# Kernel optimization log

Hardware: AMD Instinct MI355X
Metric: run time of the kernel (lower is better)

## Reference

```python
import jax, jax.numpy as jnp
import numpy as np


def setup_inputs() -> dict:
    key = jax.random.key(0)
    k1, k2, k3, k4 = jax.random.split(key, 4)
    B, C, H, W = 8, 512, 64, 64  # h must equal w per the broadcast in the original
    opt = jax.random.normal(k1, (B, C, H, W), dtype=jnp.float32)
    sar = jax.random.normal(k2, (B, C, H, W), dtype=jnp.float32)
    # 1x1 conv weights, shape [out_c, in_c] (kernel spatial dims are 1x1)
    W_opt = jax.random.normal(k3, (C, C), dtype=jnp.float32) * (2.0 / C) ** 0.5
    W_sar = jax.random.normal(k4, (C, C), dtype=jnp.float32) * (2.0 / C) ** 0.5
    return {"opt": opt, "sar": sar, "W_opt": W_opt, "W_sar": W_sar}


def _branch(x, Wc):
    # 1x1 conv: per-pixel channel mixing. Q = K = V (same conv applied to same input).
    f = jnp.einsum('oc,bchw->bohw', Wc, x)            # (b,c,h,w)
    # S[b,c,i,j] = sum_h Q[b,c,h,i] * K[b,c,h,j]  (transpose(2,3) @ original)
    S = jnp.einsum('bchi,bchj->bcij', f, f)           # (b,c,w,w)
    # nn.Softmax() with no dim on 4D -> softmax over channel dim (axis=1)
    S = jax.nn.softmax(S, axis=1)
    return f, S


def reference(opt, sar, W_opt, W_sar):
    V_opt, S_opt = _branch(opt, W_opt)
    V_sar, S_sar = _branch(sar, W_sar)
    hadamard = S_opt * S_sar                          # (b,c,w,w); h==w lets it broadcast with V
    Att = (V_opt * hadamard) * (V_sar * hadamard)
    return Att
```

## Files before the change

kernel.cpp:

```cpp
#include <hip/hip_runtime.h>
#include <cstdint>

#define CCH 512
#define HW  4096
#define WDIM 64
#define NBATCH 8
#define CHW ((size_t)CCH * HW)

typedef __attribute__((ext_vector_type(8))) short bf16x8;
typedef __attribute__((ext_vector_type(4))) float f32x4;

__device__ __forceinline__ unsigned short f2bf(float x) {
  unsigned u = __float_as_uint(x);
  unsigned r = (u + 0x7FFFu + ((u >> 16) & 1u)) >> 16;
  return (unsigned short)r;
}
__device__ __forceinline__ float bf2f(unsigned short h) {
  return __uint_as_float(((unsigned)h) << 16);
}

__device__ __forceinline__ void gl_lds16(const void* g, void* l) {
  __builtin_amdgcn_global_load_lds(
      (const __attribute__((address_space(1))) void*)g,
      (__attribute__((address_space(3))) void*)l, 16, 0, 0);
}

__global__ __launch_bounds__(256) void wsplit_k(
    const float* __restrict__ Wo, const float* __restrict__ Wsr,
    unsigned short* __restrict__ Whl) {
  const int br = blockIdx.y;
  const float* W = br ? Wsr : Wo;
  const int i = blockIdx.x * 256 + threadIdx.x;
  const float x = W[i];
  const unsigned short h = f2bf(x);
  unsigned short* dst = Whl + (size_t)br * 524288;
  dst[i] = h;
  dst[262144 + i] = f2bf(x - bf2f(h));
}

__global__ __launch_bounds__(256, 4) void mfma_conv_k(
    const unsigned short* __restrict__ Whl,
    const float* __restrict__ opt, const float* __restrict__ sar,
    float* __restrict__ F, int b0) {
  const int z = blockIdx.z;
  const int br = z & 1, bl = z >> 1;
  const unsigned short* Ah_g = Whl + (size_t)br * 524288;
  const unsigned short* Al_g = Ah_g + 262144;
  const float* Xb = (br ? sar : opt) + (size_t)(b0 + bl) * CHW;
  const int n0 = blockIdx.x * 128, m0 = blockIdx.y * 128;

  __shared__ unsigned short Ahs[128 * 32];
  __shared__ unsigned short Als[128 * 32];
  __shared__ float Xs[32 * 128];

  const int tid = threadIdx.x;
  const int wave = tid >> 6, lane = tid & 63;
  const int wm = (wave >> 1) * 64, wn = (wave & 1) * 64;

  f32x4 acc[4][4] = {};

  const int rl = lane >> 2;
  const int kcA = (((lane & 3) ^ ((lane >> 3) & 3)) * 8);

  const int brow_off = wave * 2 + (lane >> 5);
  const int bcol = (lane & 31) * 4;

  const int fr = lane & 15;
  const int quad = lane >> 4;
  const int khA = ((quad ^ ((lane >> 1) & 3)) * 8);

  for (int k0 = 0; k0 < CCH; k0 += 32) {
    __syncthreads();
#pragma unroll
    for (int q = 0; q < 2; ++q) {
      const int rbase = wave * 32 + q * 16;
      const int r = rbase + rl;
      gl_lds16(Ah_g + (size_t)(m0 + r) * CCH + k0 + kcA, &Ahs[rbase * 32]);
      gl_lds16(Al_g + (size_t)(m0 + r) * CCH + k0 + kcA, &Als[rbase * 32]);
    }
#pragma unroll
    for (int t = 0; t < 4; ++t) {
      const int row = t * 8 + brow_off;
      const int srccol = (bcol + 128 - 8 * t) & 127;
      gl_lds16(&Xb[(size_t)(k0 + row) * HW + n0 + srccol],
               &Xs[t * 1024 + wave * 256]);
    }
    __syncthreads();

    bf16x8 ah[4], al[4];
#pragma unroll
    for (int i = 0; i < 4; ++i) {
      ah[i] = *(const bf16x8*)&Ahs[(wm + i * 16 + fr) * 32 + khA];
      al[i] = *(const bf16x8*)&Als[(wm + i * 16 + fr) * 32 + khA];
    }

#pragma unroll
    for (int j = 0; j < 4; ++j) {
      const int colj = (wn + j * 16 + fr + 8 * quad) & 127;
      unsigned short hs[8], ls[8];
#pragma unroll
      for (int s = 0; s < 8; ++s) {
        const float x = Xs[(quad * 8 + s) * 128 + colj];
        const unsigned xu = __float_as_uint(x);
        const float hi = __uint_as_float(xu & 0xFFFF0000u);
        const float lof = x - hi;
        hs[s] = (unsigned short)(xu >> 16);
        ls[s] = (unsigned short)(__float_as_uint(lof) >> 16);
      }
      const bf16x8 bh = *(const bf16x8*)hs;
      const bf16x8 bl = *(const bf16x8*)ls;
#pragma unroll
      for (int i = 0; i < 4; ++i) {
        acc[i][j] = __builtin_amdgcn_mfma_f32_16x16x32_bf16(ah[i], bh, acc[i][j], 0, 0, 0);
        acc[i][j] = __builtin_amdgcn_mfma_f32_16x16x32_bf16(ah[i], bl, acc[i][j], 0, 0, 0);
        acc[i][j] = __builtin_amdgcn_mfma_f32_16x16x32_bf16(al[i], bh, acc[i][j], 0, 0, 0);
      }
    }
  }

  float* Fb = F + (size_t)z * CHW;
  const int col = lane & 15, rq = (lane >> 4) * 4;
#pragma unroll
  for (int i = 0; i < 4; ++i)
#pragma unroll
    for (int j = 0; j < 4; ++j) {
      const int n = n0 + wn + j * 16 + col;
#pragma unroll
      for (int r = 0; r < 4; ++r) {
        const int m = m0 + wm + i * 16 + rq + r;
        Fb[(size_t)m * HW + n] = acc[i][j][r];
      }
    }
}

#define FT_S 72
__global__ __launch_bounds__(256, 4) void gram_k(
    const float* __restrict__ F, float* __restrict__ S) {
  const size_t base = ((size_t)blockIdx.y * CCH + blockIdx.x) * HW;
  const float* Fc = F + base;
  float* Sc = S + base;

  __shared__ float Fs[64][68];
  __shared__ unsigned short FtH[64 * FT_S];
  __shared__ unsigned short FtL[64 * FT_S];

  const int tid = threadIdx.x;

  {
    const int h = tid >> 2;
    const int w0 = (tid & 3) * 16;
    const float* src = &Fc[h * 64 + w0];
    float4 v0 = *(const float4*)(src + 0);
    float4 v1 = *(const float4*)(src + 4);
    float4 v2 = *(const float4*)(src + 8);
    float4 v3 = *(const float4*)(src + 12);
    *(float4*)&Fs[h][w0 + 0]  = v0;
    *(float4*)&Fs[h][w0 + 4]  = v1;
    *(float4*)&Fs[h][w0 + 8]  = v2;
    *(float4*)&Fs[h][w0 + 12] = v3;
  }
  __syncthreads();

  {
    const int w = tid & 63;
    const int hc = (tid >> 6) * 16;
    unsigned short hb[16], lb[16];
#pragma unroll
    for (int k = 0; k < 16; ++k) {
      const float x = Fs[hc + k][w];
      const unsigned short h = f2bf(x);
      hb[k] = h;
      lb[k] = f2bf(x - bf2f(h));
    }
    unsigned short* dh = &FtH[w * FT_S + hc];
    unsigned short* dl = &FtL[w * FT_S + hc];
    *(uint4*)(dh + 0) = *(uint4*)&hb[0];
    *(uint4*)(dh + 8) = *(uint4*)&hb[8];
    *(uint4*)(dl + 0) = *(uint4*)&lb[0];
    *(uint4*)(dl + 8) = *(uint4*)&lb[8];
  }
  __syncthreads();

  const int wave = tid >> 6, lane = tid & 63;
  const int wm = (wave >> 1) * 32, wn = (wave & 1) * 32;
  const int fr = lane & 15, kq = (lane >> 4) * 8;

  f32x4 acc[2][2] = {};
#pragma unroll
  for (int kcc = 0; kcc < 2; ++kcc) {
    bf16x8 ah[2], al[2], bh[2], bl[2];
#pragma unroll
    for (int i = 0; i < 2; ++i) {
      ah[i] = *(const bf16x8*)&FtH[(wm + i * 16 + fr) * FT_S + kcc * 32 + kq];
      al[i] = *(const bf16x8*)&FtL[(wm + i * 16 + fr) * FT_S + kcc * 32 + kq];
      bh[i] = *(const bf16x8*)&FtH[(wn + i * 16 + fr) * FT_S + kcc * 32 + kq];
      bl[i] = *(const bf16x8*)&FtL[(wn + i * 16 + fr) * FT_S + kcc * 32 + kq];
    }
#pragma unroll
    for (int i = 0; i < 2; ++i)
#pragma unroll
      for (int j = 0; j < 2; ++j) {
        acc[i][j] = __builtin_amdgcn_mfma_f32_16x16x32_bf16(ah[i], bh[j], acc[i][j], 0, 0, 0);
        acc[i][j] = __builtin_amdgcn_mfma_f32_16x16x32_bf16(ah[i], bl[j], acc[i][j], 0, 0, 0);
        acc[i][j] = __builtin_amdgcn_mfma_f32_16x16x32_bf16(al[i], bh[j], acc[i][j], 0, 0, 0);
      }
  }

  const int rq = (lane >> 4) * 4;
#pragma unroll
  for (int i = 0; i < 2; ++i)
#pragma unroll
    for (int j = 0; j < 2; ++j) {
      const int n = wn + j * 16 + fr;
#pragma unroll
      for (int r = 0; r < 4; ++r) {
        const int m = wm + i * 16 + rq + r;
        Sc[m * 64 + n] = acc[i][j][r];
      }
    }
}

__global__ __launch_bounds__(1024, 8) void softmax_fuse_k(
    const float* __restrict__ S, const float* __restrict__ Fbuf,
    float* __restrict__ Out) {
  const int i = blockIdx.x;
  const int b = blockIdx.y;
  const int tid = threadIdx.x;
  const int jl = (tid & 15) * 4;
  const int g = tid >> 4;

  const size_t rowO = (size_t)(b * 2) * CHW + (size_t)i * WDIM;
  const size_t rowS = rowO + CHW;

  float mo[4], lo[4], ms[4], ls[4];
#pragma unroll
  for (int k = 0; k < 4; ++k) { mo[k] = -1e30f; lo[k] = 0.f; ms[k] = -1e30f; ls[k] = 0.f; }

#pragma unroll
  for (int cc = 0; cc < 8; ++cc) {
    const int c = g * 8 + cc;
    const size_t off = (size_t)c * HW + jl;
    float4 xo = *(const float4*)&S[rowO + off];
    float4 xs = *(const float4*)&S[rowS + off];
    float xov[4] = {xo.x, xo.y, xo.z, xo.w};
    float xsv[4] = {xs.x, xs.y, xs.z, xs.w};
#pragma unroll
    for (int k = 0; k < 4; ++k) {
      float nm = fmaxf(mo[k], xov[k]);
      lo[k] = lo[k] * __expf(mo[k] - nm) + __expf(xov[k] - nm);
      mo[k] = nm;
      nm = fmaxf(ms[k], xsv[k]);
      ls[k] = ls[k] * __expf(ms[k] - nm) + __expf(xsv[k] - nm);
      ms[k] = nm;
    }
  }

  __shared__ float sm[2][64][64];
  __shared__ float sl[2][64][64];
  __shared__ float Mf[2][64];
  __shared__ float Li[2][64];

  *(float4*)&sm[0][g][jl] = make_float4(mo[0], mo[1], mo[2], mo[3]);
  *(float4*)&sl[0][g][jl] = make_float4(lo[0], lo[1], lo[2], lo[3]);
  *(float4*)&sm[1][g][jl] = make_float4(ms[0], ms[1], ms[2], ms[3]);
  *(float4*)&sl[1][g][jl] = make_float4(ls[0], ls[1], ls[2], ls[3]);
  __syncthreads();

  if (tid < 128) {
    const int br = tid >> 6, j = tid & 63;
    float M = -1e30f;
#pragma unroll 16
    for (int t = 0; t < 64; ++t) M = fmaxf(M, sm[br][t][j]);
    float L = 0.f;
#pragma unroll 16
    for (int t = 0; t < 64; ++t) L += sl[br][t][j] * __expf(sm[br][t][j] - M);
    Mf[br][j] = M;
    Li[br][j] = 1.f / L;
  }
  __syncthreads();

  float4 Mo4 = *(const float4*)&Mf[0][jl];
  float4 iLo4 = *(const float4*)&Li[0][jl];
  float4 Ms4 = *(const float4*)&Mf[1][jl];
  float4 iLs4 = *(const float4*)&Li[1][jl];
  float Mov[4] = {Mo4.x, Mo4.y, Mo4.z, Mo4.w};
  float iLov[4] = {iLo4.x, iLo4.y, iLo4.z, iLo4.w};
  float Msv[4] = {Ms4.x, Ms4.y, Ms4.z, Ms4.w};
  float iLsv[4] = {iLs4.x, iLs4.y, iLs4.z, iLs4.w};

#pragma unroll
  for (int cc = 0; cc < 8; ++cc) {
    const int c = g * 8 + cc;
    const size_t off = (size_t)c * HW + jl;
    float4 xo = *(const float4*)&S[rowO + off];
    float4 xs = *(const float4*)&S[rowS + off];
    float4 fo = *(const float4*)&Fbuf[rowO + off];
    float4 fs = *(const float4*)&Fbuf[rowS + off];
    float xov[4] = {xo.x, xo.y, xo.z, xo.w};
    float xsv[4] = {xs.x, xs.y, xs.z, xs.w};
    float fov[4] = {fo.x, fo.y, fo.z, fo.w};
    float fsv[4] = {fs.x, fs.y, fs.z, fs.w};
    float ov[4];
#pragma unroll
    for (int k = 0; k < 4; ++k) {
      const float ho = __expf(xov[k] - Mov[k]) * iLov[k];
      const float hs = __expf(xsv[k] - Msv[k]) * iLsv[k];
      float h2 = ho * hs;
      h2 *= h2;
      ov[k] = fov[k] * fsv[k] * h2;
    }
    *(float4*)&Out[(size_t)b * CHW + (size_t)c * HW + (size_t)i * WDIM + jl] =
        make_float4(ov[0], ov[1], ov[2], ov[3]);
  }
}

extern "C" void kernel_launch(void* const* d_in, const int* in_sizes, int n_in,
                              void* d_out, int out_size, void* d_ws, size_t ws_size,
                              hipStream_t stream) {
  const float* opt = (const float*)d_in[0];
  const float* sar = (const float*)d_in[1];
  const float* Wo  = (const float*)d_in[2];
  const float* Wsr = (const float*)d_in[3];
  float* out = (float*)d_out;

  unsigned short* Whl = (unsigned short*)d_ws;
  const size_t whlElems = 2u * 2u * 262144u;
  const size_t perBl = 2 * CHW;
  const size_t perBlBytes = perBl * 8;
  int bc = (int)((ws_size - whlElems * 2) / perBlBytes);
  if (bc < 1) bc = 1;
  if (bc > NBATCH) bc = NBATCH;
  const int passes = (NBATCH + bc - 1) / bc;
  const int nbp = (NBATCH + passes - 1) / passes;

  float* Fbuf = (float*)(Whl + whlElems);
  float* Sbuf = Fbuf + (size_t)bc * perBl;

  hipLaunchKernelGGL(wsplit_k, dim3(1024, 2), dim3(256), 0, stream, Wo, Wsr, Whl);

  for (int b0 = 0; b0 < NBATCH; b0 += nbp) {
    const int nb = (NBATCH - b0 < nbp) ? (NBATCH - b0) : nbp;

    hipLaunchKernelGGL(mfma_conv_k, dim3(32, 4, nb * 2), dim3(256), 0, stream,
                       Whl, opt, sar, Fbuf, b0);

    hipLaunchKernelGGL(gram_k, dim3(CCH, nb * 2), dim3(256), 0, stream,
                       Fbuf, Sbuf);

    hipLaunchKernelGGL(softmax_fuse_k, dim3(WDIM, nb), dim3(1024), 0, stream,
                       Sbuf, Fbuf, out + (size_t)b0 * CHW);
  }
}
```

Baseline: 395.2 us.

## Cache softmax inputs in registers and load gram tiles directly to LDS

The softmax kernel keeps each thread's 8 float4 score values per branch in registers instead of reading S from global memory twice. It also swaps the online max/sum update for a two-pass local max then exp-sum, which removes the rescaling exponentials. The launch-bounds occupancy hint drops from 8 to 4 so the extra 64 registers fit. In the gram kernel, the F tile is copied into an unpadded LDS buffer with global_load_lds instead of going through registers, which may raise LDS bank conflicts during the transposed reads.

```diff
diff --git a/kernel.cpp b/kernel.cpp
--- a/kernel.cpp
+++ b/kernel.cpp
@@ -140,34 +140,27 @@
   const float* Fc = F + base;
   float* Sc = S + base;
 
-  __shared__ float Fs[64][68];
+  __shared__ float Fs[64 * 64];
   __shared__ unsigned short FtH[64 * FT_S];
   __shared__ unsigned short FtL[64 * FT_S];
 
   const int tid = threadIdx.x;
+  const int wave = tid >> 6, lane = tid & 63;
+
+#pragma unroll
+  for (int t = 0; t < 4; ++t) {
+    const int off = (wave * 4 + t) * 256;
+    gl_lds16(Fc + off + lane * 4, &Fs[off]);
+  }
+  __syncthreads();
 
   {
-    const int h = tid >> 2;
-    const int w0 = (tid & 3) * 16;
-    const float* src = &Fc[h * 64 + w0];
-    float4 v0 = *(const float4*)(src + 0);
-    float4 v1 = *(const float4*)(src + 4);
-    float4 v2 = *(const float4*)(src + 8);
-    float4 v3 = *(const float4*)(src + 12);
-    *(float4*)&Fs[h][w0 + 0]  = v0;
-    *(float4*)&Fs[h][w0 + 4]  = v1;
-    *(float4*)&Fs[h][w0 + 8]  = v2;
-    *(float4*)&Fs[h][w0 + 12] = v3;
-  }
-  __syncthreads();
-
-  {
-    const int w = tid & 63;
-    const int hc = (tid >> 6) * 16;
+    const int w = lane;
+    const int hc = wave * 16;
     unsigned short hb[16], lb[16];
 #pragma unroll
     for (int k = 0; k < 16; ++k) {
-      const float x = Fs[hc + k][w];
+      const float x = Fs[(hc + k) * 64 + w];
       const unsigned short h = f2bf(x);
       hb[k] = h;
       lb[k] = f2bf(x - bf2f(h));
@@ -181,7 +174,6 @@
   }
   __syncthreads();
 
-  const int wave = tid >> 6, lane = tid & 63;
   const int wm = (wave >> 1) * 32, wn = (wave & 1) * 32;
   const int fr = lane & 15, kq = (lane >> 4) * 8;
 
@@ -220,7 +212,7 @@
     }
 }
 
-__global__ __launch_bounds__(1024, 8) void softmax_fuse_k(
+__global__ __launch_bounds__(1024, 4) void softmax_fuse_k(
     const float* __restrict__ S, const float* __restrict__ Fbuf,
     float* __restrict__ Out) {
   const int i = blockIdx.x;
@@ -232,27 +224,28 @@
   const size_t rowO = (size_t)(b * 2) * CHW + (size_t)i * WDIM;
   const size_t rowS = rowO + CHW;
 
+  float4 xoc[8], xsc[8];
   float mo[4], lo[4], ms[4], ls[4];
 #pragma unroll
-  for (int k = 0; k < 4; ++k) { mo[k] = -1e30f; lo[k] = 0.f; ms[k] = -1e30f; ls[k] = 0.f; }
+  for (int k = 0; k < 4; ++k) { mo[k] = -1e30f; ms[k] = -1e30f; lo[k] = 0.f; ls[k] = 0.f; }
 
 #pragma unroll
   for (int cc = 0; cc < 8; ++cc) {
     const int c = g * 8 + cc;
     const size_t off = (size_t)c * HW + jl;
-    float4 xo = *(const float4*)&S[rowO + off];
-    float4 xs = *(const float4*)&S[rowS + off];
-    float xov[4] = {xo.x, xo.y, xo.z, xo.w};
-    float xsv[4] = {xs.x, xs.y, xs.z, xs.w};
-#pragma unroll
-    for (int k = 0; k < 4; ++k) {
-      float nm = fmaxf(mo[k], xov[k]);
-      lo[k] = lo[k] * __expf(mo[k] - nm) + __expf(xov[k] - nm);
-      mo[k] = nm;
-      nm = fmaxf(ms[k], xsv[k]);
-      ls[k] = ls[k] * __expf(ms[k] - nm) + __expf(xsv[k] - nm);
-      ms[k] = nm;
-    }
+    xoc[cc] = *(const float4*)&S[rowO + off];
+    xsc[cc] = *(const float4*)&S[rowS + off];
+    mo[0] = fmaxf(mo[0], xoc[cc].x); mo[1] = fmaxf(mo[1], xoc[cc].y);
+    mo[2] = fmaxf(mo[2], xoc[cc].z); mo[3] = fmaxf(mo[3], xoc[cc].w);
+    ms[0] = fmaxf(ms[0], xsc[cc].x); ms[1] = fmaxf(ms[1], xsc[cc].y);
+    ms[2] = fmaxf(ms[2], xsc[cc].z); ms[3] = fmaxf(ms[3], xsc[cc].w);
+  }
+#pragma unroll
+  for (int cc = 0; cc < 8; ++cc) {
+    lo[0] += __expf(xoc[cc].x - mo[0]); lo[1] += __expf(xoc[cc].y - mo[1]);
+    lo[2] += __expf(xoc[cc].z - mo[2]); lo[3] += __expf(xoc[cc].w - mo[3]);
+    ls[0] += __expf(xsc[cc].x - ms[0]); ls[1] += __expf(xsc[cc].y - ms[1]);
+    ls[2] += __expf(xsc[cc].z - ms[2]); ls[3] += __expf(xsc[cc].w - ms[3]);
   }
 
   __shared__ float sm[2][64][64];
@@ -292,12 +285,10 @@
   for (int cc = 0; cc < 8; ++cc) {
     const int c = g * 8 + cc;
     const size_t off = (size_t)c * HW + jl;
-    float4 xo = *(const float4*)&S[rowO + off];
-    float4 xs = *(const float4*)&S[rowS + off];
     float4 fo = *(const float4*)&Fbuf[rowO + off];
     float4 fs = *(const float4*)&Fbuf[rowS + off];
-    float xov[4] = {xo.x, xo.y, xo.z, xo.w};
-    float xsv[4] = {xs.x, xs.y, xs.z, xs.w};
+    float xov[4] = {xoc[cc].x, xoc[cc].y, xoc[cc].z, xoc[cc].w};
+    float xsv[4] = {xsc[cc].x, xsc[cc].y, xsc[cc].z, xsc[cc].w};
     float fov[4] = {fo.x, fo.y, fo.z, fo.w};
     float fsv[4] = {fs.x, fs.y, fs.z, fs.w};
     float ov[4];
```

Measured after the change: 358.7 us. 9.2% less time.
